# Kernel tuning notes

Measured on AMD Instinct MI355X. Metric: run time of the kernel, lower is better.

Reference implementation:

```python
import jax, jax.numpy as jnp
import numpy as np

B, CQ, CKV, LQ, LKV, HEADS = 4, 1024, 1024, 2048, 2048, 16


def _conv1x1(W, x):
    # Conv1d with kernel size 1: out[b,o,l] = sum_i W[o,i] * x[b,i,l]
    return jnp.einsum('oi,bil->bol', W, x)


def _linear_interp(x, L_out):
    # F.interpolate(mode='linear', align_corners=False) on (B,C,L)
    B_, C_, L_in = x.shape
    if L_in == L_out:
        return x
    scale = L_in / L_out
    pos = (jnp.arange(L_out, dtype=x.dtype) + 0.5) * scale - 0.5
    pos = jnp.clip(pos, 0.0, L_in - 1)
    lo = jnp.floor(pos).astype(jnp.int32)
    hi = jnp.minimum(lo + 1, L_in - 1)
    w = (pos - lo.astype(x.dtype))
    return x[:, :, lo] * (1.0 - w) + x[:, :, hi] * w


def setup_inputs() -> dict:
    key = jax.random.key(0)
    ks = jax.random.split(key, 7)
    winit = 1.0 / np.sqrt(CQ)
    return {
        'query': jax.random.normal(ks[0], (B, CQ, LQ), dtype=jnp.float32),
        'context': jax.random.normal(ks[1], (B, CKV, LKV), dtype=jnp.float32),
        'Wq': jax.random.normal(ks[2], (CQ, CQ), dtype=jnp.float32) * winit,
        'Wk': jax.random.normal(ks[3], (CQ, CKV), dtype=jnp.float32) * winit,
        'Wv': jax.random.normal(ks[4], (CQ, CKV), dtype=jnp.float32) * winit,
        'Wo': jax.random.normal(ks[5], (CQ, CQ), dtype=jnp.float32) * winit,
        'bo': jnp.zeros((CQ,), dtype=jnp.float32),
        'heads': HEADS,
    }


def reference(query, context, Wq, Wk, Wv, Wo, bo, heads):
    B_, Cq, Lq = query.shape
    H = heads
    D = Cq // H
    scale = D ** (-0.5)
    q = _conv1x1(Wq, query).reshape(B_, H, D, Lq)
    k = _conv1x1(Wk, context)
    v = _conv1x1(Wv, context)
    if k.shape[2] != Lq:
        k = _linear_interp(k, Lq)
        v = _linear_interp(v, Lq)
    k = k.reshape(B_, H, D, Lq)
    v = v.reshape(B_, H, D, Lq)
    attn = jnp.einsum('bhdi,bhdj->bhij', q, k) * scale
    attn = jax.nn.softmax(attn, axis=-1)
    out = jnp.einsum('bhij,bhdj->bhdi', attn, v).reshape(B_, Cq, Lq)
    return _conv1x1(Wo, out) + bo[None, :, None] + query
```

## Files before the change

kernel.cpp:

```cpp
#include <hip/hip_runtime.h>
#include <hip/hip_bf16.h>

typedef __bf16 bf16;
typedef __attribute__((ext_vector_type(8))) __bf16 bf16x8;
typedef __attribute__((ext_vector_type(4))) __bf16 bf16x4;
typedef __attribute__((ext_vector_type(4))) float f32x4;
typedef __attribute__((ext_vector_type(8))) float f32x8;
typedef __attribute__((ext_vector_type(16))) float f32x16;
typedef unsigned int uint2v __attribute__((ext_vector_type(2)));

#define B_ 4
#define C_ 1024
#define L_ 2048
#define H_ 16
#define D_ 64

__device__ __forceinline__ int swz(int row, int g) {
    return row * 64 + (((g ^ row) & 7) << 3);
}

__device__ __forceinline__ void async_ld16(const bf16* g, bf16* l) {
    __builtin_amdgcn_global_load_lds(
        (const __attribute__((address_space(1))) unsigned int*)g,
        (__attribute__((address_space(3))) unsigned int*)l, 16, 0, 0);
}

__device__ __forceinline__ float fast_exp2(float x) {
    float r;
    asm("v_exp_f32 %0, %1" : "=v"(r) : "v"(x));
    return r;
}

__global__ void cvt_w4(const float* __restrict__ wq, const float* __restrict__ wk,
                       const float* __restrict__ wv, const float* __restrict__ wo,
                       bf16* __restrict__ oq, bf16* __restrict__ ok,
                       bf16* __restrict__ ov, bf16* __restrict__ oo,
                       float qscale) {
    int z = blockIdx.y;
    const float* in = (z == 0) ? wq : (z == 1) ? wk : (z == 2) ? wv : wo;
    bf16* out       = (z == 0) ? oq : (z == 1) ? ok : (z == 2) ? ov : oo;
    float scale     = (z == 0) ? qscale : 1.0f;
    int i = (blockIdx.x * blockDim.x + threadIdx.x) * 4;
    f32x4 x = *(const f32x4*)&in[i];
    bf16x4 y;
#pragma unroll
    for (int e = 0; e < 4; e++) y[e] = (bf16)(x[e] * scale);
    *(bf16x4*)&out[i] = y;
}

__global__ void transpose_cvt2(const float* __restrict__ q,
                               const float* __restrict__ c,
                               bf16* __restrict__ qo, bf16* __restrict__ co,
                               int nb) {
    __shared__ bf16 s[32][33];
    int z  = blockIdx.z;
    const float* pin;
    bf16* pout;
    if (z < nb) { pin = q + (size_t)z * C_ * L_;        pout = qo + (size_t)z * L_ * C_; }
    else        { pin = c + (size_t)(z - nb) * C_ * L_; pout = co + (size_t)(z - nb) * L_ * C_; }
    int c0 = blockIdx.x * 32;
    int r0 = blockIdx.y * 32;
#pragma unroll
    for (int k = 0; k < 4; k++) {
        int r = r0 + threadIdx.y + k * 8;
        s[threadIdx.y + k * 8][threadIdx.x] = (bf16)pin[(size_t)r * L_ + c0 + threadIdx.x];
    }
    __syncthreads();
#pragma unroll
    for (int k = 0; k < 4; k++) {
        int cc = c0 + threadIdx.y + k * 8;
        pout[(size_t)cc * C_ + r0 + threadIdx.x] = s[threadIdx.x][threadIdx.y + k * 8];
    }
}

__global__ __launch_bounds__(256) void gemm_fused3(const bf16* __restrict__ qT,
                                                   const bf16* __restrict__ ctxT,
                                                   const bf16* __restrict__ Wq,
                                                   const bf16* __restrict__ Wk,
                                                   const bf16* __restrict__ Wv,
                                                   bf16* __restrict__ qP,
                                                   bf16* __restrict__ kP,
                                                   bf16* __restrict__ vP,
                                                   int nb) {
    __shared__ __align__(16) bf16 smem[4 * 128 * 64];

    int seg = blockIdx.y;
    int r   = blockIdx.x;
    int cpx = nb << 4;
    int lg  = (r & 7) * cpx + (r >> 3);

    const bf16 *aP, *bP;
    bf16* dP;
    int S;
    if (seg == 0) {
        int m_idx = lg >> 3, n_idx = lg & 7;
        aP = qT + (size_t)m_idx * 128 * C_;
        bP = Wq + (size_t)n_idx * 128 * C_;
        dP = qP + (size_t)m_idx * 128 * C_ + n_idx * 128;
        S = C_;
    } else if (seg == 1) {
        int m_idx = lg >> 3, n_idx = lg & 7;
        aP = ctxT + (size_t)m_idx * 128 * C_;
        bP = Wk + (size_t)n_idx * 128 * C_;
        dP = kP + (size_t)m_idx * 128 * C_ + n_idx * 128;
        S = C_;
    } else {
        int m_idx = lg & 7;
        int nt    = lg >> 3;
        int zb    = nt >> 4;
        int nc0   = (nt & 15) * 128;
        aP = Wv + (size_t)m_idx * 128 * C_;
        bP = ctxT + (size_t)nt * 128 * C_;
        dP = vP + (size_t)zb * C_ * L_ + (size_t)m_idx * 128 * L_ + nc0;
        S = L_;
    }

    int t = threadIdx.x;
    int lane = t & 63, wave = t >> 6;
    int l15 = lane & 15, quad = lane >> 4;
    int wm = (wave >> 1) * 64, wn = (wave & 1) * 64;

    f32x4 acc[4][4];
#pragma unroll
    for (int i = 0; i < 4; i++)
#pragma unroll
        for (int j = 0; j < 4; j++) {
            f32x4 z = {0.f, 0.f, 0.f, 0.f};
            acc[i][j] = z;
        }

    int r8 = lane >> 3;
    int gl = (((lane & 7) ^ r8) & 7) * 8;
    const bf16* aG = aP + (size_t)(wave * 32 + r8) * C_ + gl;
    const bf16* wG = bP + (size_t)(wave * 32 + r8) * C_ + gl;

    auto STAGE = [&](int buf, int kk) {
        bf16* Ab = smem + buf * 8192;
        bf16* Wb = smem + 16384 + buf * 8192;
#pragma unroll
        for (int p = 0; p < 4; p++) {
            async_ld16(aG + kk + (size_t)p * 8 * C_, &Ab[(wave * 32 + p * 8) * 64]);
            async_ld16(wG + kk + (size_t)p * 8 * C_, &Wb[(wave * 32 + p * 8) * 64]);
        }
    };

    STAGE(0, 0);
    const int KT = C_ >> 6;
    for (int it = 0; it < KT; ++it) {
        int cur = it & 1;
        if (it + 1 < KT) {
            STAGE(cur ^ 1, (it + 1) << 6);
            asm volatile("s_waitcnt vmcnt(8)" ::: "memory");
        } else {
            asm volatile("s_waitcnt vmcnt(0)" ::: "memory");
        }
        __builtin_amdgcn_s_barrier();
        asm volatile("" ::: "memory");
        const bf16* Ab = smem + cur * 8192;
        const bf16* Wb = smem + 16384 + cur * 8192;
#pragma unroll
        for (int ks = 0; ks < 2; ks++) {
            bf16x8 af[4], bfr[4];
#pragma unroll
            for (int i = 0; i < 4; i++)
                af[i] = *(const bf16x8*)&Ab[swz(wm + i * 16 + l15, ks * 4 + quad)];
#pragma unroll
            for (int i = 0; i < 4; i++)
                bfr[i] = *(const bf16x8*)&Wb[swz(wn + i * 16 + l15, ks * 4 + quad)];
#pragma unroll
            for (int mt = 0; mt < 4; mt++)
#pragma unroll
                for (int nt2 = 0; nt2 < 4; nt2++)
                    acc[mt][nt2] = __builtin_amdgcn_mfma_f32_16x16x32_bf16(
                        af[mt], bfr[nt2], acc[mt][nt2], 0, 0, 0);
        }
        asm volatile("" ::: "memory");
        __builtin_amdgcn_s_barrier();
    }
    __syncthreads();

    bf16 (*Ts2)[136] = (bf16 (*)[136])smem;
#pragma unroll
    for (int mt = 0; mt < 4; mt++)
#pragma unroll
        for (int nt2 = 0; nt2 < 4; nt2++)
#pragma unroll
            for (int rr = 0; rr < 4; rr++)
                Ts2[wm + mt * 16 + quad * 4 + rr][wn + nt2 * 16 + l15] =
                    (bf16)acc[mt][nt2][rr];
    __syncthreads();
#pragma unroll
    for (int j = 0; j < 8; j++) {
        int idx = t + 256 * j;
        int ml  = idx >> 4;
        int nl8 = (idx & 15) * 8;
        bf16x8 x = *(const bf16x8*)&Ts2[ml][nl8];
        *(bf16x8*)&dP[(size_t)ml * S + nl8] = x;
    }
}

__global__ __launch_bounds__(256) void gemm_o_final(const bf16* __restrict__ A_,
                                                    const bf16* __restrict__ Wt,
                                                    const float* __restrict__ query_,
                                                    const float* __restrict__ bo,
                                                    float* __restrict__ out_,
                                                    int nb) {
    __shared__ __align__(16) bf16 smem[4 * 128 * 64];

    int bid = blockIdx.x;
    int cpx = nb << 4;
    int lg  = (bid & 7) * cpx + (bid >> 3);
    int m   = lg >> 3;
    int n0  = (lg & 7) * 128;
    int zb  = m >> 4;
    int l0  = (m & 15) * 128;

    const bf16* A      = A_ + (size_t)m * 128 * C_;
    const float* query = query_ + (size_t)zb * C_ * L_;
    float* out         = out_   + (size_t)zb * C_ * L_;

    int t = threadIdx.x;
    int lane = t & 63, wave = t >> 6;
    int l15 = lane & 15, quad = lane >> 4;
    int wm = (wave >> 1) * 64, wn = (wave & 1) * 64;

    f32x4 acc[4][4];
#pragma unroll
    for (int i = 0; i < 4; i++)
#pragma unroll
        for (int j = 0; j < 4; j++) {
            f32x4 z = {0.f, 0.f, 0.f, 0.f};
            acc[i][j] = z;
        }

    int r8 = lane >> 3;
    int gl = (((lane & 7) ^ r8) & 7) * 8;
    const bf16* aG = A  + (size_t)(wave * 32 + r8) * C_ + gl;
    const bf16* wG = Wt + (size_t)(n0 + wave * 32 + r8) * C_ + gl;

    auto STAGE = [&](int buf, int kk) {
        bf16* Ab = smem + buf * 8192;
        bf16* Wb = smem + 16384 + buf * 8192;
#pragma unroll
        for (int p = 0; p < 4; p++) {
            async_ld16(aG + kk + (size_t)p * 8 * C_, &Ab[(wave * 32 + p * 8) * 64]);
            async_ld16(wG + kk + (size_t)p * 8 * C_, &Wb[(wave * 32 + p * 8) * 64]);
        }
    };

    STAGE(0, 0);
    const int KT = C_ >> 6;
    for (int it = 0; it < KT; ++it) {
        int cur = it & 1;
        if (it + 1 < KT) {
            STAGE(cur ^ 1, (it + 1) << 6);
            asm volatile("s_waitcnt vmcnt(8)" ::: "memory");
        } else {
            asm volatile("s_waitcnt vmcnt(0)" ::: "memory");
        }
        __builtin_amdgcn_s_barrier();
        asm volatile("" ::: "memory");
        const bf16* Ab = smem + cur * 8192;
        const bf16* Wb = smem + 16384 + cur * 8192;
#pragma unroll
        for (int ks = 0; ks < 2; ks++) {
            bf16x8 af[4], bfr[4];
#pragma unroll
            for (int i = 0; i < 4; i++)
                af[i] = *(const bf16x8*)&Ab[swz(wm + i * 16 + l15, ks * 4 + quad)];
#pragma unroll
            for (int i = 0; i < 4; i++)
                bfr[i] = *(const bf16x8*)&Wb[swz(wn + i * 16 + l15, ks * 4 + quad)];
#pragma unroll
            for (int mt = 0; mt < 4; mt++)
#pragma unroll
                for (int nt = 0; nt < 4; nt++)
                    acc[mt][nt] = __builtin_amdgcn_mfma_f32_16x16x32_bf16(
                        af[mt], bfr[nt], acc[mt][nt], 0, 0, 0);
        }
        asm volatile("" ::: "memory");
        __builtin_amdgcn_s_barrier();
    }
    __syncthreads();

    bf16 (*Ts)[136] = (bf16 (*)[136])smem;
#pragma unroll
    for (int mt = 0; mt < 4; mt++)
#pragma unroll
        for (int nt = 0; nt < 4; nt++)
#pragma unroll
            for (int rr = 0; rr < 4; rr++)
                Ts[wn + nt * 16 + l15][wm + mt * 16 + quad * 4 + rr] = (bf16)acc[mt][nt][rr];
    __syncthreads();
#pragma unroll
    for (int j = 0; j < 8; j++) {
        int idx = t + 256 * j;
        int cl  = idx >> 4;
        int ll8 = (idx & 15) * 8;
        int c   = n0 + cl;
        size_t goff = (size_t)c * L_ + l0 + ll8;
        bf16x8 y = *(const bf16x8*)&Ts[cl][ll8];
        f32x8 q = *(const f32x8*)&query[goff];
        float bias = bo[c];
        f32x8 o;
#pragma unroll
        for (int e = 0; e < 8; e++)
            o[e] = (float)y[e] + bias + q[e];
        *(f32x8*)&out[goff] = o;
    }
}

__global__ __launch_bounds__(256) void flash_attn(const bf16* qT,
                                                  const bf16* __restrict__ kT,
                                                  const bf16* __restrict__ v,
                                                  bf16* oT) {
    __shared__ __align__(16) bf16 Ks[3][64 * 64];
    __shared__ __align__(16) bf16 Vs[3][64 * 64];
    int bid = blockIdx.x;
    int cpx = gridDim.x >> 3;
    int logical = (bid & 7) * cpx + (bid >> 3);
    int i0 = (logical & 15) * 128;
    int g  = logical >> 4;
    int h  = g & 15;
    int zb = g >> 4;
    int t = threadIdx.x, lane = t & 63, wave = t >> 6;
    int l31 = lane & 31, kh = lane >> 5;

    const bf16* qB = qT + (size_t)zb * L_ * C_ + (size_t)h * D_;
    const bf16* kB = kT + (size_t)zb * L_ * C_ + (size_t)h * D_;
    const bf16* vB = v  + (size_t)zb * C_ * L_ + (size_t)h * D_ * L_;
    bf16* oB       = oT + (size_t)zb * L_ * C_ + (size_t)h * D_;

    bf16x8 qf[4];
#pragma unroll
    for (int kt = 0; kt < 4; kt++)
        qf[kt] = *(const bf16x8*)&qB[(size_t)(i0 + wave * 32 + l31) * C_ +
                                     kt * 16 + kh * 8];

    f32x16 acc_o[2];
#pragma unroll
    for (int dt = 0; dt < 2; dt++)
#pragma unroll
        for (int r = 0; r < 16; r++) acc_o[dt][r] = 0.f;
    f32x16 acc_l;
#pragma unroll
    for (int r = 0; r < 16; r++) acc_l[r] = 0.f;
    f32x16 z16;
#pragma unroll
    for (int r = 0; r < 16; r++) z16[r] = 0.f;

    bf16x8 onesf;
#pragma unroll
    for (int e = 0; e < 8; e++) onesf[e] = (bf16)1.0f;

    int r8 = lane >> 3;
    int gl = (((lane & 7) ^ r8) & 7) * 8;
    const bf16* kG = kB + (size_t)(wave * 16 + r8) * C_ + gl;
    const bf16* vG = vB + (size_t)(wave * 16 + r8) * L_ + gl;

    auto STAGE = [&](int buf, int j0n) {
#pragma unroll
        for (int p = 0; p < 2; p++) {
            async_ld16(kG + (size_t)j0n * C_ + (size_t)p * 8 * C_,
                       &Ks[buf][(wave * 16 + p * 8) * 64]);
            async_ld16(vG + j0n + (size_t)p * 8 * L_,
                       &Vs[buf][(wave * 16 + p * 8) * 64]);
        }
    };

    auto QK = [&](const bf16* kb, f32x16* sout) {
#pragma unroll
        for (int jt = 0; jt < 2; jt++) {
            f32x16 s;
            {
                bf16x8 a = *(const bf16x8*)&kb[swz(jt * 32 + l31, kh)];
                s = __builtin_amdgcn_mfma_f32_32x32x16_bf16(a, qf[0], z16, 0, 0, 0);
            }
#pragma unroll
            for (int kt = 1; kt < 4; kt++) {
                bf16x8 a = *(const bf16x8*)&kb[swz(jt * 32 + l31, kt * 2 + kh)];
                s = __builtin_amdgcn_mfma_f32_32x32x16_bf16(a, qf[kt], s, 0, 0, 0);
            }
            sout[jt] = s;
        }
    };

    auto SMPV = [&](const f32x16* sin, const bf16* vb) {
#pragma unroll
        for (int jt = 0; jt < 2; jt++) {
            unsigned w[4][2];
#pragma unroll
            for (int q = 0; q < 4; q++)
#pragma unroll
                for (int c = 0; c < 2; c++) {
                    float p0 = fast_exp2(sin[jt][q * 4 + 2 * c]);
                    float p1 = fast_exp2(sin[jt][q * 4 + 2 * c + 1]);
                    asm("v_cvt_pk_bf16_f32 %0, %1, %2"
                        : "=v"(w[q][c]) : "v"(p0), "v"(p1));
                }
#pragma unroll
            for (int kp = 0; kp < 2; kp++) {
                int ks = jt * 2 + kp;
                uint2v r0 = __builtin_amdgcn_permlane32_swap(
                    w[kp * 2][0], w[kp * 2 + 1][0], false, false);
                uint2v r1 = __builtin_amdgcn_permlane32_swap(
                    w[kp * 2][1], w[kp * 2 + 1][1], false, false);
                union { unsigned u[4]; bf16x8 v8; } af;
                af.u[0] = r0[0]; af.u[1] = r1[0];
                af.u[2] = r0[1]; af.u[3] = r1[1];
#pragma unroll
                for (int dt = 0; dt < 2; dt++) {
                    bf16x8 b = *(const bf16x8*)&vb[swz(dt * 32 + l31, ks * 2 + kh)];
                    acc_o[dt] = __builtin_amdgcn_mfma_f32_32x32x16_bf16(
                        af.v8, b, acc_o[dt], 0, 0, 0);
                }
                acc_l = __builtin_amdgcn_mfma_f32_32x32x16_bf16(
                    af.v8, onesf, acc_l, 0, 0, 0);
            }
        }
    };

    const int NT = L_ / 64;
    f32x16 sb0[2], sb1[2];

    STAGE(0, 0);
    STAGE(1, 64);
    asm volatile("s_waitcnt vmcnt(4)" ::: "memory");
    __builtin_amdgcn_s_barrier();
    asm volatile("" ::: "memory");
    QK(&Ks[0][0], sb0);

    int cb = 0, nbf = 1, sbf = 2;
    auto TILE_FULL = [&](int it, f32x16* scur, f32x16* snext) {
        STAGE(sbf, (it + 2) * 64);
        asm volatile("s_waitcnt vmcnt(4)" ::: "memory");
        __builtin_amdgcn_s_barrier();
        asm volatile("" ::: "memory");
        __builtin_amdgcn_s_setprio(1);
        QK(&Ks[nbf][0], snext);
        __builtin_amdgcn_s_setprio(0);
        SMPV(scur, &Vs[cb][0]);
        asm volatile("" ::: "memory");
        __builtin_amdgcn_s_barrier();
        int t0 = cb; cb = nbf; nbf = sbf; sbf = t0;
    };

    for (int it = 0; it < NT - 2; it += 2) {
        TILE_FULL(it, sb0, sb1);
        TILE_FULL(it + 1, sb1, sb0);
    }
    {
        asm volatile("s_waitcnt vmcnt(0)" ::: "memory");
        __builtin_amdgcn_s_barrier();
        asm volatile("" ::: "memory");
        __builtin_amdgcn_s_setprio(1);
        QK(&Ks[nbf][0], sb1);
        __builtin_amdgcn_s_setprio(0);
        SMPV(sb0, &Vs[cb][0]);
        int t0 = cb; cb = nbf; nbf = sbf; sbf = t0;
    }
    SMPV(sb1, &Vs[cb][0]);

    float inv[16];
#pragma unroll
    for (int r = 0; r < 16; r++) inv[r] = __builtin_amdgcn_rcpf(acc_l[r]);
#pragma unroll
    for (int dt = 0; dt < 2; dt++)
#pragma unroll
        for (int q = 0; q < 4; q++)
#pragma unroll
            for (int r = 0; r < 4; r++) {
                int row = i0 + wave * 32 + 8 * q + 4 * kh + r;
                oB[(size_t)row * C_ + dt * 32 + l31] =
                    (bf16)(acc_o[dt][q * 4 + r] * inv[q * 4 + r]);
            }
}

extern "C" void kernel_launch(void* const* d_in, const int* in_sizes, int n_in,
                              void* d_out, int out_size, void* d_ws, size_t ws_size,
                              hipStream_t stream) {
    const float* query   = (const float*)d_in[0];
    const float* context = (const float*)d_in[1];
    const float* Wq = (const float*)d_in[2];
    const float* Wk = (const float*)d_in[3];
    const float* Wv = (const float*)d_in[4];
    const float* Wo = (const float*)d_in[5];
    const float* bo = (const float*)d_in[6];
    float* out = (float*)d_out;

    const size_t Sw = (size_t)C_ * C_;
    size_t need_batched = (4 * Sw + 3 * (size_t)B_ * L_ * C_) * sizeof(bf16);
    int nb = (ws_size >= need_batched) ? B_ : 1;

    const size_t Sslot = (size_t)nb * L_ * C_;
    bf16* WqB = (bf16*)d_ws;
    bf16* WkB = WqB + Sw;
    bf16* WvB = WkB + Sw;
    bf16* WoB = WvB + Sw;
    bf16* slotA = WoB + Sw;
    bf16* slotB = slotA + Sslot;
    bf16* slotC = slotB + Sslot;

    cvt_w4<<<dim3((unsigned)(Sw / 4 / 256), 4), 256, 0, stream>>>(
        Wq, Wk, Wv, Wo, WqB, WkB, WvB, WoB, 0.1803368801111204f);

    dim3 tb(32, 8);

    for (int b0 = 0; b0 < B_; b0 += nb) {
        const float* qx = query   + (size_t)b0 * C_ * L_;
        const float* cx = context + (size_t)b0 * C_ * L_;
        float* ob       = out     + (size_t)b0 * C_ * L_;

        bf16* vscr  = (bf16*)ob;
        bf16* ctxTs = (bf16*)ob + Sslot;

        transpose_cvt2<<<dim3(L_ / 32, C_ / 32, 2 * nb), tb, 0, stream>>>(
            qx, cx, slotA, ctxTs, nb);
        gemm_fused3<<<dim3(128 * nb, 3), 256, 0, stream>>>(
            slotA, ctxTs, WqB, WkB, WvB, slotB, slotC, vscr, nb);
        flash_attn<<<256 * nb, 256, 0, stream>>>(slotB, slotC, vscr, slotB);
        gemm_o_final<<<128 * nb, 256, 0, stream>>>(slotB, WoB, qx, bo, ob, nb);
    }
}
```

Before: 296.3 us.

## Switch flash attention K/V staging from triple to double buffering

```diff
diff --git a/kernel.cpp b/kernel.cpp
--- a/kernel.cpp
+++ b/kernel.cpp
@@ -314,8 +314,8 @@
                                                   const bf16* __restrict__ kT,
                                                   const bf16* __restrict__ v,
                                                   bf16* oT) {
-    __shared__ __align__(16) bf16 Ks[3][64 * 64];
-    __shared__ __align__(16) bf16 Vs[3][64 * 64];
+    __shared__ __align__(16) bf16 Ks[2][64 * 64];
+    __shared__ __align__(16) bf16 Vs[2][64 * 64];
     int bid = blockIdx.x;
     int cpx = gridDim.x >> 3;
     int logical = (bid & 7) * cpx + (bid >> 3);
@@ -359,13 +359,10 @@
     const bf16* vG = vB + (size_t)(wave * 16 + r8) * L_ + gl;
 
     auto STAGE = [&](int buf, int j0n) {
-#pragma unroll
-        for (int p = 0; p < 2; p++) {
-            async_ld16(kG + (size_t)j0n * C_ + (size_t)p * 8 * C_,
-                       &Ks[buf][(wave * 16 + p * 8) * 64]);
-            async_ld16(vG + j0n + (size_t)p * 8 * L_,
-                       &Vs[buf][(wave * 16 + p * 8) * 64]);
-        }
+        async_ld16(kG + (size_t)j0n * C_,              &Ks[buf][(wave * 16) * 64]);
+        async_ld16(kG + (size_t)j0n * C_ + 8 * C_,     &Ks[buf][(wave * 16 + 8) * 64]);
+        async_ld16(vG + j0n,                           &Vs[buf][(wave * 16) * 64]);
+        async_ld16(vG + j0n + (size_t)8 * L_,          &Vs[buf][(wave * 16 + 8) * 64]);
     };
 
     auto QK = [&](const bf16* kb, f32x16* sout) {
@@ -430,36 +427,31 @@
     asm volatile("" ::: "memory");
     QK(&Ks[0][0], sb0);
 
-    int cb = 0, nbf = 1, sbf = 2;
-    auto TILE_FULL = [&](int it, f32x16* scur, f32x16* snext) {
-        STAGE(sbf, (it + 2) * 64);
-        asm volatile("s_waitcnt vmcnt(4)" ::: "memory");
+    auto BODY = [&](int it, f32x16* scur, f32x16* snext) {
+        if (it + 1 < NT) {
+            asm volatile("s_waitcnt vmcnt(2)" ::: "memory");
+        } else {
+            asm volatile("s_waitcnt vmcnt(0)" ::: "memory");
+        }
         __builtin_amdgcn_s_barrier();
         asm volatile("" ::: "memory");
-        __builtin_amdgcn_s_setprio(1);
-        QK(&Ks[nbf][0], snext);
-        __builtin_amdgcn_s_setprio(0);
-        SMPV(scur, &Vs[cb][0]);
-        asm volatile("" ::: "memory");
-        __builtin_amdgcn_s_barrier();
-        int t0 = cb; cb = nbf; nbf = sbf; sbf = t0;
+        if (it + 1 < NT) {
+            __builtin_amdgcn_s_setprio(1);
+            QK(&Ks[(it + 1) & 1][0], snext);
+            __builtin_amdgcn_s_setprio(0);
+        }
+        SMPV(scur, &Vs[it & 1][0]);
+        if (it + 2 < NT) {
+            asm volatile("" ::: "memory");
+            __builtin_amdgcn_s_barrier();
+            STAGE(it & 1, (it + 2) * 64);
+        }
     };
 
-    for (int it = 0; it < NT - 2; it += 2) {
-        TILE_FULL(it, sb0, sb1);
-        TILE_FULL(it + 1, sb1, sb0);
-    }
-    {
-        asm volatile("s_waitcnt vmcnt(0)" ::: "memory");
-        __builtin_amdgcn_s_barrier();
-        asm volatile("" ::: "memory");
-        __builtin_amdgcn_s_setprio(1);
-        QK(&Ks[nbf][0], sb1);
-        __builtin_amdgcn_s_setprio(0);
-        SMPV(sb0, &Vs[cb][0]);
-        int t0 = cb; cb = nbf; nbf = sbf; sbf = t0;
-    }
-    SMPV(sb1, &Vs[cb][0]);
+    for (int it = 0; it < NT; it += 2) {
+        BODY(it, sb0, sb1);
+        BODY(it + 1, sb1, sb0);
+    }
 
     float inv[16];
 #pragma unroll
```

After: 298.2 us. About the same (+0.6%).
